# Optimization experiments

Measured on AMD Instinct MI355X. Metric: run time of the kernel, lower is better.

Reference implementation:

```python
import jax, jax.numpy as jnp
from jax import lax
import numpy as np

KS = 8        # window size
SS = 4        # shift size = KS // 2
HEADS = 4


def _l2n(t, axis):
    # torch F.normalize: x / clamp(||x||_2, min=eps)
    return t / jnp.maximum(jnp.linalg.norm(t, axis=axis, keepdims=True), 1e-12)


def _to_windows(t, heads, ks):
    # 'b (head c) (h kh) (w kw) -> b head (h w) (kh kw) c'
    b, hc, H, W = t.shape
    c = hc // heads
    hW, wW = H // ks, W // ks
    t = t.reshape(b, heads, c, hW, ks, wW, ks)
    t = t.transpose(0, 1, 3, 5, 4, 6, 2)  # b,h,hW,wW,kh,kw,c
    return t.reshape(b, heads, hW * wW, ks * ks, c)


def _from_windows(t, hW, wW, ks):
    # 'b head (h w) (kh kw) c -> b (head c) (h kh) (w kw)'
    b, heads, nW, kk, c = t.shape
    t = t.reshape(b, heads, hW, wW, ks, ks, c)
    t = t.transpose(0, 1, 6, 2, 4, 3, 5)  # b,h,c,hW,kh,wW,kw
    return t.reshape(b, heads * c, hW * ks, wW * ks)


def _talk_conv(attn, w, hW, wW):
    # Conv3d(heads->heads, kernel (3,3,1), padding same) over the (hW, wW, K)
    # grid; kernel size 1 on K means an independent 2D conv per K slot, so we
    # fold K into the batch dim and run a single 2D conv.
    b, heads, nW, a1, a2 = attn.shape
    K = a1 * a2
    t = attn.reshape(b, heads, hW, wW, K).transpose(0, 4, 1, 2, 3)
    t = t.reshape(b * K, heads, hW, wW)
    t = lax.conv_general_dilated(t, w, (1, 1), 'SAME',
                                 dimension_numbers=('NCHW', 'OIHW', 'NCHW'))
    t = t.reshape(b, K, heads, hW, wW).transpose(0, 2, 3, 4, 1)
    return t.reshape(b, heads, nW, a1, a2)


def _shift_mask(H, W, ks, ss):
    # Swin-style shifted-window mask; pure numpy constant (shapes are static).
    img = np.zeros((H, W), np.float32)
    cnt = 0
    for hs in (slice(0, -ks), slice(-ks, -ss), slice(-ss, None)):
        for ws in (slice(0, -ks), slice(-ks, -ss), slice(-ss, None)):
            img[hs, ws] = cnt
            cnt += 1
    win = img.reshape(H // ks, ks, W // ks, ks).transpose(0, 2, 1, 3).reshape(-1, ks * ks)
    diff = win[:, None, :] - win[:, :, None]
    return jnp.asarray(np.where(diff != 0, -100.0, 0.0).astype(np.float32))


def _forward(x, w_quz, w_kv, temperature, r_talking, g_talking,
             b_talking_w, l_talking_w, dw_u_w, project_w, project_out_w,
             sca_w, sca_b):
    b, c, H, W = x.shape
    hW, wW = H // KS, W // KS
    quz = jnp.einsum('oc,bchw->bohw', w_quz, x)
    q, u, z = jnp.split(quz, 3, axis=1)
    kv = jnp.einsum('oc,bchw->bohw', w_kv, x)
    k, v = jnp.split(kv, 2, axis=1)
    # shift = True
    q, k, v = (jnp.roll(t, (-SS, -SS), axis=(-1, -2)) for t in (q, k, v))
    q, k, v = (_to_windows(t, HEADS, KS) for t in (q, k, v))  # b,h,nW,kk,c
    qb, ql, qg, qr = jnp.split(q, 4, axis=-1)
    kb, kl, kg, kr = jnp.split(k, 4, axis=-1)
    vb, vl, vg, vr = jnp.split(v, 4, axis=-1)
    qb, kb = _l2n(qb, -1), _l2n(kb, -1)
    ql, kl = _l2n(ql, -2), _l2n(kl, -2)
    qg, kg = _l2n(qg, -3), _l2n(kg, -3)
    qr, kr = _l2n(qr, -3), _l2n(kr, -3)
    # 4 branches (n=window index, i/j=position-in-window, c/d=per-branch chan)
    attn_b = jnp.einsum('bhnic,bhnjc->bhnij', qb, kb) * temperature[0]
    attn_l = jnp.einsum('bhnic,bhnid->bhncd', ql, kl) * temperature[1]
    attn_g = jnp.einsum('bhnic,bhnid->bhicd', qg, kg) * temperature[2]
    attn_r = jnp.einsum('bhnic,bhnjc->bhcij', qr, kr) * temperature[3]
    # talking heads
    attn_b = _talk_conv(attn_b, b_talking_w, hW, wW)
    attn_l = _talk_conv(attn_l, l_talking_w, hW, wW)
    attn_g = jnp.einsum('hklt,bhkcd->btlcd', g_talking, attn_g)
    attn_r = jnp.einsum('hcdt,bhcij->btdij', r_talking, attn_r)
    # shifted-window mask on the brightness branch
    attn_b = attn_b + _shift_mask(H, W, KS, SS)[None, None]
    attn_b, attn_l, attn_g, attn_r = (jax.nn.softmax(t, axis=-1)
                                      for t in (attn_b, attn_l, attn_g, attn_r))
    # outputs, all arranged to (b,h,n,i,c) before un-windowing
    out_b = jnp.einsum('bhnij,bhnjc->bhnic', attn_b, vb)
    out_l = jnp.einsum('bhncd,bhnid->bhnic', attn_l, vl)
    out_g = jnp.einsum('bhicd,bhnid->bhnic', attn_g, vg)
    out_r = jnp.einsum('bhcij,bhnjc->bhnic', attn_r, vr)
    out = jnp.concatenate([_from_windows(t, hW, wW, KS)
                           for t in (out_b, out_l, out_g, out_r)], axis=1)
    out = jnp.roll(out, (SS, SS), axis=(-1, -2))
    # simplified channel attention (global avg pool + 1x1 conv with bias)
    s = jnp.mean(out, axis=(2, 3))
    s = jnp.einsum('oc,bc->bo', sca_w, s) + sca_b
    out = jnp.einsum('oc,bchw->bohw', project_w, out * s[:, :, None, None])
    dw = lax.conv_general_dilated(u, dw_u_w, (1, 1), 'SAME',
                                  feature_group_count=u.shape[1],
                                  dimension_numbers=('NCHW', 'OIHW', 'NCHW'))
    out = out + dw
    return jnp.einsum('oc,bchw->bohw', project_out_w, out * z)


def setup_inputs() -> dict:
    key = jax.random.key(0)
    ks = jax.random.split(key, 12)
    dim, h_dim = 64, 128
    cd = h_dim // HEADS // 4
    b, H, W = 4, 192, 192
    r = lambda i, shp, s: jax.random.normal(ks[i], shp, jnp.float32) * s
    return {
        'x': jax.random.normal(ks[0], (b, dim, H, W), jnp.float32),
        'w_quz': r(1, (3 * h_dim, dim), 0.1),
        'w_kv': r(2, (2 * h_dim, dim), 0.1),
        'temperature': jnp.ones((4, HEADS, 1, 1, 1), jnp.float32),
        'r_talking': r(3, (HEADS, cd, cd, HEADS), 0.2),
        'g_talking': r(4, (HEADS, KS * KS, KS * KS, HEADS), 0.05),
        'b_talking_w': r(5, (HEADS, HEADS, 3, 3), 0.2),
        'l_talking_w': r(6, (HEADS, HEADS, 3, 3), 0.2),
        'dw_u_w': r(7, (h_dim, 1, 3, 3), 0.2),
        'project_w': r(8, (h_dim, h_dim), 0.08),
        'project_out_w': r(9, (dim, h_dim), 0.08),
        'sca_w': r(10, (h_dim, h_dim), 0.08),
        'sca_b': jnp.zeros((h_dim,), jnp.float32),
    }


def reference(x, w_quz, w_kv, temperature, r_talking, g_talking,
              b_talking_w, l_talking_w, dw_u_w, project_w, project_out_w,
              sca_w, sca_b):
    return _forward(x, w_quz, w_kv, temperature, r_talking, g_talking,
                    b_talking_w, l_talking_w, dw_u_w, project_w,
                    project_out_w, sca_w, sca_b)
```

## Files before the change

kernel.cpp:

```cpp
#include <hip/hip_runtime.h>
#include <hip/hip_fp16.h>
#include <cstdint>
#include <cstddef>

#define BB   4
#define CIN  64
#define HD   128
#define NH   4
#define CHW  32
#define CB   8
#define IMG  192
#define SSH  4
#define NWS  24
#define NWIN 576
#define KK   64
#define HWP  (IMG*IMG)

static const size_t NQK16  = (size_t)NH*NWIN*KK*16;
static const size_t NV32   = (size_t)NH*NWIN*KK*CHW;
static const size_t NGR    = (size_t)NH*KK*NWIN*CB;
static const size_t NSP    = (size_t)HD*HWP;
static const size_t NATTNB = (size_t)NH*NWIN*KK*KK;
static const size_t NATTNL = (size_t)NH*NWIN*64;
static const size_t NATTNG = (size_t)NH*KK*64;
static const size_t NATTNR = (size_t)NH*CB*KK*KK;
static const size_t NPART  = (size_t)8*NATTNR;

__device__ inline float wave_max(float v){
  #pragma unroll
  for (int s=1;s<64;s<<=1) v = fmaxf(v, __shfl_xor(v, s));
  return v;
}
__device__ inline float wave_sum(float v){
  #pragma unroll
  for (int s=1;s<64;s<<=1) v += __shfl_xor(v, s);
  return v;
}
__device__ inline float g8_max(float v){
  v = fmaxf(v, __shfl_xor(v,1)); v = fmaxf(v, __shfl_xor(v,2)); v = fmaxf(v, __shfl_xor(v,4));
  return v;
}
__device__ inline float g8_sum(float v){
  v += __shfl_xor(v,1); v += __shfl_xor(v,2); v += __shfl_xor(v,4);
  return v;
}
__device__ inline int regionc(int y){ return (y < IMG-8) ? 0 : ((y < IMG-4) ? 1 : 2); }

__device__ inline size_t widx(int h,int n,int i,int c){
  return (((size_t)h*NWIN + n)*KK + i)*CHW + c;
}
__device__ inline size_t widx16(int h,int n,int i,int c){
  return (((size_t)h*NWIN + n)*KK + i)*16 + c;
}
__device__ inline size_t gidx(int h,int i,int n,int c){
  return (((size_t)(h*KK + i))*NWIN + n)*CB + c;
}
__device__ inline size_t ridx(int h,int c,int n,int i){
  return (((size_t)(h*CB + c))*NWIN + n)*KK + i;
}

__global__ __launch_bounds__(256) void k1_proj(
    const float* __restrict__ x, const float* __restrict__ wquz, const float* __restrict__ wkv,
    float* __restrict__ qw, float* __restrict__ kw, float* __restrict__ vw,
    float* __restrict__ qg, float* __restrict__ kg,
    float* __restrict__ qr, float* __restrict__ kr,
    float* __restrict__ u, float* __restrict__ zbuf, int bsel)
{
  __shared__ float xs[64][20];
  __shared__ float tb[128][17];
  int blk = blockIdx.x;
  int xc = blk % 12, y = blk / 12;
  int x0 = xc*16;
  int t = threadIdx.x;
  {
    int c = t >> 2, p4 = (t & 3)*4;
    float4 v = *(const float4*)&x[((size_t)(bsel*CIN+c)*IMG + y)*IMG + x0 + p4];
    *(float4*)&xs[c][p4] = v;
  }
  int py  = (y + IMG - SSH) % IMG;
  int kh  = py & 7, hwq = py >> 3;
  int wwA = ((x0 - SSH + IMG) % IMG) >> 3;
  int wwB = x0 >> 3;
  int wwC = (x0 + 8) >> 3;
  int pnA = hwq*NWS + wwA, pnB = hwq*NWS + wwB, pnC = hwq*NWS + wwC;
  int piA = kh*8 + 4, piB = kh*8, piC = kh*8;
  #define PN_(p) ((p)<4 ? pnA : ((p)<12 ? pnB : pnC))
  #define PI_(p) ((p)<4 ? (piA+(p)) : ((p)<12 ? (piB+(p)-4) : (piC+(p)-12)))
  __syncthreads();

  int o;
  if (t < 64)       o = (t>>4)*32 + (t&15);
  else if (t < 96)  o = ((t-64)>>3)*32 + 16 + (t&7);
  else if (t < 128) o = ((t-96)>>3)*32 + 24 + (t&7);
  else              o = t;

  {
    const float* wr = wquz + (size_t)o*CIN;
    float acc[16];
    #pragma unroll
    for (int p = 0; p < 16; ++p) acc[p] = 0.f;
    for (int cc = 0; cc < 64; cc += 4){
      float4 w4 = *(const float4*)(wr + cc);
      #pragma unroll
      for (int p = 0; p < 16; ++p){
        acc[p] += w4.x * xs[cc  ][p];
        acc[p] += w4.y * xs[cc+1][p];
        acc[p] += w4.z * xs[cc+2][p];
        acc[p] += w4.w * xs[cc+3][p];
      }
    }
    if (t < 64){
      int h = t >> 4, c = t & 15;
      #pragma unroll
      for (int p = 0; p < 16; ++p) qw[widx16(h,PN_(p),PI_(p),c)] = acc[p];
    } else if (t < 96){
      int h = (t-64) >> 3, cg = t & 7;
      #pragma unroll
      for (int p = 0; p < 16; ++p) qg[gidx(h,PI_(p),PN_(p),cg)] = acc[p];
    } else if (t < 128){
      int h = (t-96) >> 3, cr = t & 7;
      *(float4*)&qr[ridx(h,cr,pnA,piA)]   = make_float4(acc[0],acc[1],acc[2],acc[3]);
      *(float4*)&qr[ridx(h,cr,pnB,piB)]   = make_float4(acc[4],acc[5],acc[6],acc[7]);
      *(float4*)&qr[ridx(h,cr,pnB,piB+4)] = make_float4(acc[8],acc[9],acc[10],acc[11]);
      *(float4*)&qr[ridx(h,cr,pnC,piC)]   = make_float4(acc[12],acc[13],acc[14],acc[15]);
    } else {
      int ch = o - 128;
      #pragma unroll
      for (int p = 0; p < 16; ++p) tb[ch][p] = acc[p];
    }
  }
  __syncthreads();
  {
    int px = t & 15, chg = t >> 4;
    size_t ub = (size_t)y*IMG + x0 + px;
    #pragma unroll
    for (int cc = 0; cc < 8; ++cc){
      int ch = chg*8 + cc;
      u[(size_t)ch*HWP + ub] = tb[ch][px];
    }
  }

  {
    const float* wr = wkv + (size_t)o*CIN;
    float acc[16];
    #pragma unroll
    for (int p = 0; p < 16; ++p) acc[p] = 0.f;
    for (int cc = 0; cc < 64; cc += 4){
      float4 w4 = *(const float4*)(wr + cc);
      #pragma unroll
      for (int p = 0; p < 16; ++p){
        acc[p] += w4.x * xs[cc  ][p];
        acc[p] += w4.y * xs[cc+1][p];
        acc[p] += w4.z * xs[cc+2][p];
        acc[p] += w4.w * xs[cc+3][p];
      }
    }
    if (t < 64){
      int h = t >> 4, c = t & 15;
      #pragma unroll
      for (int p = 0; p < 16; ++p) kw[widx16(h,PN_(p),PI_(p),c)] = acc[p];
    } else if (t < 96){
      int h = (t-64) >> 3, cg = t & 7;
      #pragma unroll
      for (int p = 0; p < 16; ++p) kg[gidx(h,PI_(p),PN_(p),cg)] = acc[p];
    } else if (t < 128){
      int h = (t-96) >> 3, cr = t & 7;
      *(float4*)&kr[ridx(h,cr,pnA,piA)]   = make_float4(acc[0],acc[1],acc[2],acc[3]);
      *(float4*)&kr[ridx(h,cr,pnB,piB)]   = make_float4(acc[4],acc[5],acc[6],acc[7]);
      *(float4*)&kr[ridx(h,cr,pnB,piB+4)] = make_float4(acc[8],acc[9],acc[10],acc[11]);
      *(float4*)&kr[ridx(h,cr,pnC,piC)]   = make_float4(acc[12],acc[13],acc[14],acc[15]);
    } else {
      int oc = o - 128; int h = oc >> 5, c = oc & 31;
      #pragma unroll
      for (int p = 0; p < 16; ++p) vw[widx(h,PN_(p),PI_(p),c)] = acc[p];
    }
  }

  __syncthreads();
  {
    int zr = t >> 1, ph = t & 1;
    const float* wr = wquz + (size_t)(256 + zr)*CIN;
    int pb = ph*8;
    float acc[8];
    #pragma unroll
    for (int p = 0; p < 8; ++p) acc[p] = 0.f;
    for (int cc = 0; cc < 64; cc += 4){
      float4 w4 = *(const float4*)(wr + cc);
      #pragma unroll
      for (int p = 0; p < 8; ++p){
        acc[p] += w4.x * xs[cc  ][pb+p];
        acc[p] += w4.y * xs[cc+1][pb+p];
        acc[p] += w4.z * xs[cc+2][pb+p];
        acc[p] += w4.w * xs[cc+3][pb+p];
      }
    }
    #pragma unroll
    for (int p = 0; p < 8; ++p) tb[zr][pb+p] = acc[p];
  }
  __syncthreads();
  {
    int px = t & 15, chg = t >> 4;
    size_t zb = (size_t)y*IMG + x0 + px;
    #pragma unroll
    for (int cc = 0; cc < 8; ++cc){
      int ch = chg*8 + cc;
      zbuf[(size_t)ch*HWP + zb] = tb[ch][px];
    }
  }
  #undef PN_
  #undef PI_
}

__global__ __launch_bounds__(256) void kA(
    const float* __restrict__ qw, const float* __restrict__ kw,
    const float* __restrict__ qg, const float* __restrict__ kg,
    const float* __restrict__ qr, const float* __restrict__ kr,
    const float* __restrict__ temp,
    __half* __restrict__ attnB, float* __restrict__ attnL,
    float* __restrict__ attnG, float* __restrict__ part,
    float* __restrict__ invqr, float* __restrict__ invkr)
{
  __shared__ __align__(16) char smem[36864];
  int blk = blockIdx.x;
  int t = threadIdx.x;

  if (blk < 576){
    float (*qs)[64][8] = (float(*)[64][8])smem;
    int wv = t >> 6, j = t & 63;
    int gid = blk*4 + wv;
    int n = gid % NWIN, h = gid / NWIN;
    size_t base = widx16(h,n,j,0);
    float q8[CB], k8[CB];
    float sq = 0.f, sk2 = 0.f;
    #pragma unroll
    for (int c = 0; c < CB; ++c){
      q8[c] = qw[base+c]; sq += q8[c]*q8[c];
      k8[c] = kw[base+c]; sk2 += k8[c]*k8[c];
    }
    float invq = 1.f/fmaxf(sqrtf(sq),1e-12f), invk = 1.f/fmaxf(sqrtf(sk2),1e-12f);
    #pragma unroll
    for (int c = 0; c < CB; ++c){ qs[wv][j][c] = q8[c]*invq; k8[c] *= invk; }
    __syncthreads();
    float tmp = temp[h];
    __half* orow = attnB + (size_t)gid*KK*KK;
    for (int i = 0; i < KK; ++i){
      float a = 0.f;
      #pragma unroll
      for (int c = 0; c < CB; ++c) a += qs[wv][i][c]*k8[c];
      orow[(size_t)i*KK + j] = __float2half(a * tmp);
    }
  } else if (blk < 1152){
    int b2 = blk - 576;
    float (*qs)[64][8] = (float(*)[64][8])smem;
    float (*ks)[64][8] = (float(*)[64][8])(smem + 8192);
    float (*invqA)[8] = (float(*)[8])(smem + 16384);
    float (*invkA)[8] = (float(*)[8])(smem + 16384 + 128);
    int wv = t >> 6, tl = t & 63;
    int gid = b2*4 + wv;
    int n = gid % NWIN, h = gid / NWIN;
    size_t base = widx16(h,n,tl,8);
    #pragma unroll
    for (int c = 0; c < CB; ++c){ qs[wv][tl][c] = qw[base+c]; ks[wv][tl][c] = kw[base+c]; }
    __syncthreads();
    int c8 = tl & 7, ig = tl >> 3;
    float sq = 0.f, sk2 = 0.f;
    for (int i = ig; i < KK; i += 8){
      float a = qs[wv][i][c8]; sq += a*a;
      float b = ks[wv][i][c8]; sk2 += b*b;
    }
    #pragma unroll
    for (int m = 8; m < 64; m <<= 1){ sq += __shfl_xor(sq,m); sk2 += __shfl_xor(sk2,m); }
    if (tl < 8){ invqA[wv][tl] = 1.f/fmaxf(sqrtf(sq),1e-12f); invkA[wv][tl] = 1.f/fmaxf(sqrtf(sk2),1e-12f); }
    __syncthreads();
    int c = tl >> 3, d = tl & 7;
    float a = 0.f;
    for (int i = 0; i < KK; ++i) a += qs[wv][i][c]*ks[wv][i][d];
    attnL[(size_t)gid*64 + tl] = a * invqA[wv][c] * invkA[wv][d] * temp[NH + h];
  } else if (blk < 1408){
    int b2 = blk - 1152;
    int i = b2 & 63, h = b2 >> 6;
    float* sq = (float*)smem;
    float* sk = sq + 512;
    float (*redA)[64] = (float(*)[64])(smem + 4096);
    float (*redQ)[64] = (float(*)[64])(smem + 4096 + 1024);
    float (*redK)[64] = (float(*)[64])(smem + 4096 + 2048);
    size_t base = ((size_t)(h*KK+i))*NWIN*CB;
    int np = t >> 6, cd = t & 63, c = cd >> 3, d = cd & 7;
    float a = 0.f, qs2 = 0.f, ks2 = 0.f;
    for (int n0 = 0; n0 < NWIN; n0 += 64){
      __syncthreads();
      for (int idx = t; idx < 512; idx += 256){
        sq[idx] = qg[base + (size_t)n0*CB + idx];
        sk[idx] = kg[base + (size_t)n0*CB + idx];
      }
      __syncthreads();
      for (int nn = np; nn < 64; nn += 4){
        float qv = sq[nn*8+c], kv = sk[nn*8+d];
        a += qv*kv; qs2 += qv*qv; ks2 += kv*kv;
      }
    }
    __syncthreads();
    redA[np][cd] = a; redQ[np][cd] = qs2; redK[np][cd] = ks2;
    __syncthreads();
    if (t < 64){
      float at = redA[0][t]+redA[1][t]+redA[2][t]+redA[3][t];
      float qt = redQ[0][t]+redQ[1][t]+redQ[2][t]+redQ[3][t];
      float kt = redK[0][t]+redK[1][t]+redK[2][t]+redK[3][t];
      at *= (1.f/fmaxf(sqrtf(qt),1e-12f)) * (1.f/fmaxf(sqrtf(kt),1e-12f)) * temp[2*NH + h];
      attnG[(size_t)(h*KK+i)*64 + t] = at;
    }
  } else if (blk < 1664){
    int b2 = blk - 1408;
    int chunk = b2 >> 5, hc = b2 & 31;
    int n0 = chunk*72;
    float* sq = (float*)smem;
    float* sk = sq + 72*64;
    size_t base = (size_t)hc*NWIN*KK + (size_t)n0*KK;
    for (int idx = t; idx < 72*64/4; idx += 256){
      *(float4*)&sq[idx*4] = *(const float4*)&qr[base + (size_t)idx*4];
      *(float4*)&sk[idx*4] = *(const float4*)&kr[base + (size_t)idx*4];
    }
    __syncthreads();
    int j = t & 63, ig = t >> 6;
    float acc[16];
    #pragma unroll
    for (int p = 0; p < 16; ++p) acc[p] = 0.f;
    for (int nn = 0; nn < 72; ++nn){
      float kv = sk[nn*64+j];
      #pragma unroll
      for (int p = 0; p < 16; ++p) acc[p] += sq[nn*64 + ig*16 + p]*kv;
    }
    float* ob = part + (size_t)b2*4096;
    #pragma unroll
    for (int p = 0; p < 16; ++p) ob[(size_t)(ig*16+p)*64 + j] = acc[p];
  } else {
    int hc = blk - 1664;
    float (*rq)[64] = (float(*)[64])smem;
    float (*rk)[64] = (float(*)[64])(smem + 1024);
    size_t base = (size_t)hc*NWIN*KK;
    int i = t & 63, ng = t >> 6;
    float sq = 0.f, sk2 = 0.f;
    for (int n = ng; n < NWIN; n += 4){
      float a = qr[base + (size_t)n*KK + i]; sq  += a*a;
      float b = kr[base + (size_t)n*KK + i]; sk2 += b*b;
    }
    rq[ng][i] = sq; rk[ng][i] = sk2;
    __syncthreads();
    if (t < 64){
      float s = rq[0][t]+rq[1][t]+rq[2][t]+rq[3][t];
      invqr[hc*KK + t] = 1.f/fmaxf(sqrtf(s),1e-12f);
    } else if (t < 128){
      int i2 = t - 64;
      float s = rk[0][i2]+rk[1][i2]+rk[2][i2]+rk[3][i2];
      invkr[hc*KK + i2] = 1.f/fmaxf(sqrtf(s),1e-12f);
    }
  }
}

__global__ __launch_bounds__(256) void kB(
    const __half* __restrict__ attnB, const float* __restrict__ btw,
    const float* __restrict__ vw, float* __restrict__ outa,
    const float* __restrict__ attnL, const float* __restrict__ ltw,
    const float* __restrict__ attnG, const float* __restrict__ gtalk,
    float* __restrict__ attnGp,
    const float* __restrict__ part, const float* __restrict__ invqr,
    const float* __restrict__ invkr, const float* __restrict__ temp,
    float* __restrict__ attnR,
    const float* __restrict__ u, const float* __restrict__ dww,
    float* __restrict__ dwu)
{
  __shared__ __align__(16) char smem[12800];
  int blk = blockIdx.x;
  int t = threadIdx.x;

  if (blk < 9216){
    float (*pbuf)[4][66] = (float(*)[4][66])smem;
    float (*vv)[8][66]   = (float(*)[8][66])(smem + 4224);
    int ig = blk / NWIN, n = blk % NWIN;
    int i0 = ig*4;
    int hw = n / NWS, ww = n % NWS;
    int w = t >> 6, l = t & 63;
    {
      size_t vb = widx(w, n, l, 0);
      float4 va = *(const float4*)&vw[vb];
      float4 vb4 = *(const float4*)&vw[vb + 4];
      vv[w][0][l] = va.x;  vv[w][1][l] = va.y;  vv[w][2][l] = va.z;  vv[w][3][l] = va.w;
      vv[w][4][l] = vb4.x; vv[w][5][l] = vb4.y; vv[w][6][l] = vb4.z; vv[w][7][l] = vb4.w;
    }
    int i = i0 + w;
    float a0 = 0.f, a1 = 0.f, a2 = 0.f, a3 = 0.f;
    #pragma unroll
    for (int nb = 0; nb < 9; ++nb){
      const int dy = nb/3 - 1, dx = nb%3 - 1;
      int hw2 = hw + dy, ww2 = ww + dx;
      if (hw2 >= 0 && hw2 < NWS && ww2 >= 0 && ww2 < NWS){
        int n2 = hw2*NWS + ww2;
        #pragma unroll
        for (int h = 0; h < 4; ++h){
          float r = __half2float(attnB[((size_t)(h*NWIN + n2)*KK + i)*KK + l]);
          a0 += btw[(0*4 + h)*9 + nb] * r;
          a1 += btw[(1*4 + h)*9 + nb] * r;
          a2 += btw[(2*4 + h)*9 + nb] * r;
          a3 += btw[(3*4 + h)*9 + nb] * r;
        }
      }
    }
    int kh = i >> 3, kwd = i & 7;
    int cntI = regionc(hw*8 + kh)*3 + regionc(ww*8 + kwd);
    int cntJ = regionc(hw*8 + (l>>3))*3 + regionc(ww*8 + (l&7));
    float mval = (cntI != cntJ) ? -100.f : 0.f;
    a0 += mval; a1 += mval; a2 += mval; a3 += mval;
    {
      float m0 = wave_max(a0); float e0 = __expf(a0 - m0); pbuf[0][w][l] = e0 / wave_sum(e0);
      float m1 = wave_max(a1); float e1 = __expf(a1 - m1); pbuf[1][w][l] = e1 / wave_sum(e1);
      float m2 = wave_max(a2); float e2 = __expf(a2 - m2); pbuf[2][w][l] = e2 / wave_sum(e2);
      float m3 = wave_max(a3); float e3 = __expf(a3 - m3); pbuf[3][w][l] = e3 / wave_sum(e3);
    }
    __syncthreads();
    {
      int i2 = l >> 4, c = (l >> 1) & 7, jq = l & 1;
      const float* pr = &pbuf[w][i2][jq*32];
      const float* vr = &vv[w][c][jq*32];
      float s = 0.f;
      #pragma unroll
      for (int q = 0; q < 32; ++q) s += pr[q] * vr[q];
      s += __shfl_xor(s, 1);
      if (jq == 0){
        int ii = i0 + i2;
        int khh = ii >> 3, kww = ii & 7;
        int Y = (hw*8 + khh + SSH) % IMG;
        int X = (ww*8 + kww + SSH) % IMG;
        outa[((size_t)(w*CB + c)*HWP) + (size_t)Y*IMG + X] = s;
      }
    }
  } else if (blk < 9792){
    int n = blk - 9216;
    int hw = n/NWS, ww = n%NWS;
    float (*rows)[9][64] = (float(*)[9][64])smem;
    float* wt = (float*)(smem + 9216);
    float (*P)[8][8] = (float(*)[8][8])(smem + 9792);
    if (t < NH*NH*9) wt[t] = ltw[t];
    for (int l = t; l < NH*9*64; l += 256){
      int h = l/(9*64); int nb = (l/64)%9; int cd = l & 63;
      int dy = nb/3-1, dx = nb%3-1; int hw2 = hw+dy, ww2 = ww+dx;
      float v = 0.f;
      if (hw2>=0 && hw2<NWS && ww2>=0 && ww2<NWS)
        v = attnL[((size_t)h*NWIN + hw2*NWS + ww2)*64 + cd];
      rows[h][nb][cd] = v;
    }
    __syncthreads();
    int tt = t >> 6; int cd = t & 63; int c = cd >> 3, d = cd & 7;
    float a = 0.f;
    #pragma unroll
    for (int h = 0; h < NH; ++h)
      #pragma unroll
      for (int nb = 0; nb < 9; ++nb)
        a += wt[(tt*NH + h)*9 + nb] * rows[h][nb][cd];
    float m = g8_max(a);
    float e = __expf(a - m);
    P[tt][c][d] = e / g8_sum(e);
    __syncthreads();
    int i = t & 63;
    size_t vbase = widx(tt, n, i, 8);
    float vl[CB];
    #pragma unroll
    for (int d2 = 0; d2 < CB; ++d2) vl[d2] = vw[vbase + d2];
    int kh = i>>3, kwd = i&7;
    int Y = (hw*8+kh+SSH)%IMG, X = (ww*8+kwd+SSH)%IMG;
    #pragma unroll
    for (int c2 = 0; c2 < CB; ++c2){
      float o = 0.f;
      #pragma unroll
      for (int d2 = 0; d2 < CB; ++d2) o += P[tt][c2][d2]*vl[d2];
      outa[((size_t)(32 + tt*CB + c2)*IMG + Y)*IMG + X] = o;
    }
  } else if (blk < 9856){
    int bb = blk - 9792;
    int w = t >> 6, cd = t & 63;
    int idx = bb*4 + w;
    int l = idx & 63, t2 = idx >> 6;
    float a = 0.f;
    for (int h = 0; h < NH; ++h)
      for (int k = 0; k < KK; ++k)
        a += gtalk[((size_t)(h*KK + k)*KK + l)*NH + t2] * attnG[((size_t)h*KK + k)*64 + cd];
    float m = g8_max(a);
    float e = __expf(a - m);
    attnGp[((size_t)t2*KK + l)*64 + cd] = e / g8_sum(e);
  } else if (blk < 10368){
    int e = (blk - 9856)*256 + t;
    float s = 0.f;
    #pragma unroll
    for (int ch = 0; ch < 8; ++ch) s += part[(size_t)ch*NATTNR + e];
    int hc = e >> 12, ij = e & 4095, i = ij >> 6, j = ij & 63;
    attnR[e] = s * invqr[hc*64+i] * invkr[hc*64+j] * temp[3*NH + (hc>>3)];
  } else {
    int bb = blk - 10368;
    int ch = bb / 48; int y0 = (bb % 48) * 4;
    float (*rows)[192] = (float(*)[192])smem;
    for (int idx = t; idx < 6*48; idx += 256){
      int r = idx / 48, px4 = (idx % 48)*4;
      int yy = y0 - 1 + r;
      float4 v = {0.f,0.f,0.f,0.f};
      if (yy >= 0 && yy < IMG) v = *(const float4*)&u[(size_t)ch*HWP + (size_t)yy*IMG + px4];
      rows[r][px4] = v.x; rows[r][px4+1] = v.y; rows[r][px4+2] = v.z; rows[r][px4+3] = v.w;
    }
    float kw9[9];
    #pragma unroll
    for (int q = 0; q < 9; ++q) kw9[q] = dww[ch*9 + q];
    __syncthreads();
    int r = t >> 6, lane = t & 63;
    for (int kx = 0; kx < 3; ++kx){
      int px = lane + kx*64;
      float s = 0.f;
      #pragma unroll
      for (int dy = 0; dy < 3; ++dy){
        #pragma unroll
        for (int dx = -1; dx <= 1; ++dx){
          int xx = px + dx;
          if (xx >= 0 && xx < IMG) s += kw9[dy*3 + dx + 1] * rows[r+dy][xx];
        }
      }
      dwu[(size_t)ch*HWP + (size_t)(y0+r)*IMG + px] = s;
    }
  }
}

__global__ __launch_bounds__(256) void kC(
    const float* __restrict__ attnGp, const float* __restrict__ vw,
    float* __restrict__ outa,
    const float* __restrict__ attnR, const float* __restrict__ rtalk,
    float* __restrict__ attnRp)
{
  __shared__ __align__(16) char smem[16512];
  int blk = blockIdx.x;
  int t = threadIdx.x;

  if (blk < 2304){
    float* P = (float*)smem;
    int n = blk % NWIN; int t2 = blk / NWIN;
    for (int l = t; l < KK*64; l += 256) P[l] = attnGp[(size_t)t2*KK*64 + l];
    __syncthreads();
    int i = t >> 2; int c0 = (t & 3)*2;
    size_t vbase = widx(t2, n, i, 16);
    float vg[8];
    #pragma unroll
    for (int d = 0; d < 8; ++d) vg[d] = vw[vbase + d];
    int hw = n/NWS, ww = n%NWS; int kh = i>>3, kwd = i&7;
    int Y = (hw*8+kh+SSH)%IMG, X = (ww*8+kwd+SSH)%IMG;
    for (int c = c0; c < c0+2; ++c){
      float o = 0.f;
      #pragma unroll
      for (int d = 0; d < 8; ++d) o += P[(i*8 + c)*8 + d]*vg[d];
      outa[((size_t)(64 + t2*CB + c)*IMG + Y)*IMG + X] = o;
    }
  } else {
    int bb = blk - 2304;
    int d = bb % CB; int t2 = bb / CB;
    float (*S)[64] = (float(*)[64])smem;
    float* wr2 = (float*)(smem + 16384);
    if (t < 32){ int h = t >> 3, c = t & 7; wr2[t] = rtalk[((size_t)(h*CB + c)*CB + d)*NH + t2]; }
    __syncthreads();
    int j = t & 63; int ig = t >> 6;
    float acc[16];
    #pragma unroll
    for (int p = 0; p < 16; ++p) acc[p] = 0.f;
    for (int hc = 0; hc < 32; ++hc){
      float w = wr2[hc];
      const float* Ar = attnR + (size_t)hc*KK*KK;
      #pragma unroll
      for (int p = 0; p < 16; ++p) acc[p] += w * Ar[(size_t)(ig*16+p)*KK + j];
    }
    #pragma unroll
    for (int p = 0; p < 16; ++p) S[ig*16+p][j] = acc[p];
    __syncthreads();
    for (int r = ig; r < 64; r += 4){
      float a = S[r][j];
      float m = wave_max(a);
      float e = __expf(a - m);
      attnRp[(((size_t)t2*CB + d)*KK + r)*KK + j] = e / wave_sum(e);
    }
  }
}

__global__ __launch_bounds__(256) void k7c(
    const float* __restrict__ attnRp, const float* __restrict__ vw, float* __restrict__ outa)
{
  int n = blockIdx.x % NWIN; int t2 = blockIdx.x / NWIN;
  __shared__ float vr[KK][CB];
  int t = threadIdx.x;
  for (int l = t; l < KK*CB; l += 256){
    int j = l >> 3, c = l & 7;
    vr[j][c] = vw[widx(t2, n, j, 24 + c)];
  }
  __syncthreads();
  int i = t & 63; int cg = t >> 6;
  int hw = n/NWS, ww = n%NWS; int kh = i>>3, kwd = i&7;
  int Y = (hw*8+kh+SSH)%IMG, X = (ww*8+kwd+SSH)%IMG;
  for (int c = cg*2; c < cg*2+2; ++c){
    const float* Pr = attnRp + (((size_t)t2*CB + c)*KK + i)*KK;
    float o = 0.f;
    for (int j = 0; j < KK; ++j) o += Pr[j]*vr[j][c];
    outa[((size_t)(96 + t2*CB + c)*IMG + Y)*IMG + X] = o;
  }
}

__global__ __launch_bounds__(256) void k8_mean(const float* __restrict__ outa, float* __restrict__ meanb){
  int ch = blockIdx.x;
  const float4* p = (const float4*)(outa + (size_t)ch*HWP);
  float s = 0.f;
  for (int l = threadIdx.x; l < HWP/4; l += 256){
    float4 v = p[l]; s += v.x+v.y+v.z+v.w;
  }
  __shared__ float red[256];
  red[threadIdx.x] = s; __syncthreads();
  for (int k = 128; k > 0; k >>= 1){
    if (threadIdx.x < k) red[threadIdx.x] += red[threadIdx.x + k];
    __syncthreads();
  }
  if (threadIdx.x == 0) meanb[ch] = red[0] / (float)HWP;
}

#define PADX 68
__global__ __launch_bounds__(256) void k9a(
    const float* __restrict__ outa, const float* __restrict__ meanb,
    const float* __restrict__ scaw, const float* __restrict__ scab,
    const float* __restrict__ projw, const float* __restrict__ dwu,
    const float* __restrict__ zbuf, float* __restrict__ out2z)
{
  __shared__ float WT[128][128];
  __shared__ float xsv[128][PADX];
  __shared__ float sv[128];
  int t = threadIdx.x;
  if (t < 128){
    float s = scab[t];
    const float* srow = scaw + (size_t)t*HD;
    for (int c = 0; c < HD; c += 4){
      float4 w = *(const float4*)&srow[c];
      float4 mm = *(const float4*)&meanb[c];
      s += w.x*mm.x + w.y*mm.y + w.z*mm.z + w.w*mm.w;
    }
    sv[t] = s;
  }
  for (int idx = t; idx < 4096; idx += 256){
    int o = idx & 127; int c4 = (idx >> 7) * 4;
    float4 w = *(const float4*)&projw[(size_t)o*HD + c4];
    WT[c4][o] = w.x; WT[c4+1][o] = w.y; WT[c4+2][o] = w.z; WT[c4+3][o] = w.w;
  }
  int px4 = (t & 15) * 4; int og8 = (t >> 4) * 8;
  for (int tile = 0; tile < 2; ++tile){
    int tid = blockIdx.x * 2 + tile;
    int y = tid / 3, x0 = (tid % 3) * 64;
    size_t sb = (size_t)y*IMG + x0;
    __syncthreads();
    for (int idx = t; idx < 2048; idx += 256){
      int c = idx >> 4; int p4 = (idx & 15) * 4;
      float4 v = *(const float4*)&outa[(size_t)c*HWP + sb + p4];
      float s = sv[c];
      xsv[c][p4] = v.x*s; xsv[c][p4+1] = v.y*s; xsv[c][p4+2] = v.z*s; xsv[c][p4+3] = v.w*s;
    }
    __syncthreads();
    float acc[8][4];
    #pragma unroll
    for (int a = 0; a < 8; ++a){ acc[a][0]=0.f; acc[a][1]=0.f; acc[a][2]=0.f; acc[a][3]=0.f; }
    for (int c = 0; c < 128; ++c){
      float4 xv = *(const float4*)&xsv[c][px4];
      float4 wA = *(const float4*)&WT[c][og8];
      float4 wB = *(const float4*)&WT[c][og8+4];
      float w8[8] = {wA.x,wA.y,wA.z,wA.w,wB.x,wB.y,wB.z,wB.w};
      #pragma unroll
      for (int a = 0; a < 8; ++a){
        acc[a][0] += w8[a]*xv.x; acc[a][1] += w8[a]*xv.y;
        acc[a][2] += w8[a]*xv.z; acc[a][3] += w8[a]*xv.w;
      }
    }
    #pragma unroll
    for (int oo = 0; oo < 8; ++oo){
      int o = og8 + oo;
      size_t off = (size_t)o*HWP + sb + px4;
      float4 d = *(const float4*)&dwu[off];
      float4 z = *(const float4*)&zbuf[off];
      float4 r;
      r.x = (acc[oo][0]+d.x)*z.x; r.y = (acc[oo][1]+d.y)*z.y;
      r.z = (acc[oo][2]+d.z)*z.z; r.w = (acc[oo][3]+d.w)*z.w;
      *(float4*)&out2z[off] = r;
    }
  }
}

__global__ __launch_bounds__(256) void k9b(
    const float* __restrict__ out2z, const float* __restrict__ projow,
    float* __restrict__ dout, int bsel)
{
  __shared__ float WT2[128][64];
  __shared__ float xsv[128][PADX];
  int t = threadIdx.x;
  for (int idx = t; idx < 2048; idx += 256){
    int o = idx & 63; int c4 = (idx >> 6) * 4;
    float4 w = *(const float4*)&projow[(size_t)o*HD + c4];
    WT2[c4][o] = w.x; WT2[c4+1][o] = w.y; WT2[c4+2][o] = w.z; WT2[c4+3][o] = w.w;
  }
  int px4 = (t & 15) * 4; int og4 = (t >> 4) * 4;
  for (int tile = 0; tile < 2; ++tile){
    int tid = blockIdx.x * 2 + tile;
    int y = tid / 3, x0 = (tid % 3) * 64;
    size_t sb = (size_t)y*IMG + x0;
    __syncthreads();
    for (int idx = t; idx < 2048; idx += 256){
      int c = idx >> 4; int p4 = (idx & 15) * 4;
      float4 v = *(const float4*)&out2z[(size_t)c*HWP + sb + p4];
      xsv[c][p4] = v.x; xsv[c][p4+1] = v.y; xsv[c][p4+2] = v.z; xsv[c][p4+3] = v.w;
    }
    __syncthreads();
    float acc[4][4];
    #pragma unroll
    for (int a = 0; a < 4; ++a){ acc[a][0]=0.f; acc[a][1]=0.f; acc[a][2]=0.f; acc[a][3]=0.f; }
    for (int c = 0; c < 128; ++c){
      float4 xv = *(const float4*)&xsv[c][px4];
      float4 w4 = *(const float4*)&WT2[c][og4];
      float w4a[4] = {w4.x,w4.y,w4.z,w4.w};
      #pragma unroll
      for (int a = 0; a < 4; ++a){
        acc[a][0] += w4a[a]*xv.x; acc[a][1] += w4a[a]*xv.y;
        acc[a][2] += w4a[a]*xv.z; acc[a][3] += w4a[a]*xv.w;
      }
    }
    #pragma unroll
    for (int oo = 0; oo < 4; ++oo){
      int o = og4 + oo;
      float4 r; r.x = acc[oo][0]; r.y = acc[oo][1]; r.z = acc[oo][2]; r.w = acc[oo][3];
      *(float4*)&dout[(size_t)(bsel*CIN + o)*HWP + sb + px4] = r;
    }
  }
}

extern "C" void kernel_launch(void* const* d_in, const int* in_sizes, int n_in,
                              void* d_out, int out_size, void* d_ws, size_t ws_size,
                              hipStream_t stream)
{
  const float* x     = (const float*)d_in[0];
  const float* wquz  = (const float*)d_in[1];
  const float* wkv   = (const float*)d_in[2];
  const float* temp  = (const float*)d_in[3];
  const float* rtalk = (const float*)d_in[4];
  const float* gtalk = (const float*)d_in[5];
  const float* btw   = (const float*)d_in[6];
  const float* ltw   = (const float*)d_in[7];
  const float* dww   = (const float*)d_in[8];
  const float* projw = (const float*)d_in[9];
  const float* projow= (const float*)d_in[10];
  const float* scaw  = (const float*)d_in[11];
  const float* scab  = (const float*)d_in[12];
  float* dout = (float*)d_out;

  float* ws = (float*)d_ws;
  float* qw    = ws;
  float* kw    = qw + NQK16;
  float* vw    = kw + NQK16;
  float* qg    = vw + NV32;
  float* kg    = qg + NGR;
  float* qr    = kg + NGR;
  float* kr    = qr + NGR;
  float* u     = kr + NGR;
  float* zbuf  = u + NSP;
  float* outa  = zbuf + NSP;
  float* attnBf= outa + NSP;
  __half* attnBh = (__half*)attnBf;
  float* attnL = attnBf + NSP;
  float* attnG = attnL + NATTNL;
  float* attnGp= attnG + NATTNG;
  float* part  = attnGp + NATTNG;
  float* attnR = part + NPART;
  float* attnRp= attnR + NATTNR;
  float* invqr = attnRp + NATTNR;
  float* invkr = invqr + 2048;
  float* meanb = invkr + 2048;
  float* dwu   = qw;
  float* out2z = attnBf;

  for (int b = 0; b < BB; ++b){
    k1_proj<<<IMG*12, 256, 0, stream>>>(x, wquz, wkv, qw, kw, vw, qg, kg, qr, kr, u, zbuf, b);

    kA<<<1696, 256, 0, stream>>>(qw, kw, qg, kg, qr, kr, temp,
                                 attnBh, attnL, attnG, part, invqr, invkr);

    kB<<<16512, 256, 0, stream>>>(attnBh, btw, vw, outa, attnL, ltw,
                                  attnG, gtalk, attnGp, part, invqr, invkr, temp, attnR,
                                  u, dww, dwu);

    kC<<<2336, 256, 0, stream>>>(attnGp, vw, outa, attnR, rtalk, attnRp);

    k7c<<<NH*NWIN, 256, 0, stream>>>(attnRp, vw, outa);

    k8_mean<<<HD, 256, 0, stream>>>(outa, meanb);

    k9a<<<288, 256, 0, stream>>>(outa, meanb, scaw, scab, projw, dwu, zbuf, out2z);
    k9b<<<288, 256, 0, stream>>>(out2z, projow, dout, b);
  }
}
```

Baseline: 1.194 ms.

## Fuse k1 projection passes and interleave attnB heads for packed loads

The projection kernel now computes the q/k/z (or u/v) outputs in a single pass over the shared x tile, with several accumulator sets per thread, instead of three separate passes. It also drops the half-occupied z pass. The fp16 attention buffer attnB is relaid out with the head index innermost, so the talking-heads conv can fetch all four heads of one element with a single 8-byte load rather than four scattered 2-byte loads. The trade-off is higher register pressure in k1 and less coalesced strided fp16 stores when kA writes attnB.

Measured after the change: 1.320 ms. 1.11x slower.

```diff
diff --git a/kernel.cpp b/kernel.cpp
--- a/kernel.cpp
+++ b/kernel.cpp
@@ -57,6 +57,9 @@
 }
 __device__ inline size_t ridx(int h,int c,int n,int i){
   return (((size_t)(h*CB + c))*NWIN + n)*KK + i;
+}
+__device__ inline size_t bidx(int n,int i,int j,int h){
+  return ((((size_t)n*KK + i)*KK + j)*NH) + h;
 }
 
 __global__ __launch_bounds__(256) void k1_proj(
@@ -92,42 +95,60 @@
   if (t < 64)       o = (t>>4)*32 + (t&15);
   else if (t < 96)  o = ((t-64)>>3)*32 + 16 + (t&7);
   else if (t < 128) o = ((t-96)>>3)*32 + 24 + (t&7);
-  else              o = t;
-
-  {
-    const float* wr = wquz + (size_t)o*CIN;
-    float acc[16];
-    #pragma unroll
-    for (int p = 0; p < 16; ++p) acc[p] = 0.f;
+  else              o = t - 128;
+
+  float acc1[16], acc2[16], acc3[16];
+  #pragma unroll
+  for (int p = 0; p < 16; ++p){ acc1[p]=0.f; acc2[p]=0.f; acc3[p]=0.f; }
+
+  if (t < 128){
+    const float* w1 = wquz + (size_t)o*CIN;
+    const float* w2 = wkv  + (size_t)o*CIN;
+    const float* w3 = wquz + (size_t)(256+o)*CIN;
     for (int cc = 0; cc < 64; cc += 4){
-      float4 w4 = *(const float4*)(wr + cc);
-      #pragma unroll
-      for (int p = 0; p < 16; ++p){
-        acc[p] += w4.x * xs[cc  ][p];
-        acc[p] += w4.y * xs[cc+1][p];
-        acc[p] += w4.z * xs[cc+2][p];
-        acc[p] += w4.w * xs[cc+3][p];
-      }
-    }
-    if (t < 64){
-      int h = t >> 4, c = t & 15;
-      #pragma unroll
-      for (int p = 0; p < 16; ++p) qw[widx16(h,PN_(p),PI_(p),c)] = acc[p];
-    } else if (t < 96){
-      int h = (t-64) >> 3, cg = t & 7;
-      #pragma unroll
-      for (int p = 0; p < 16; ++p) qg[gidx(h,PI_(p),PN_(p),cg)] = acc[p];
-    } else if (t < 128){
-      int h = (t-96) >> 3, cr = t & 7;
-      *(float4*)&qr[ridx(h,cr,pnA,piA)]   = make_float4(acc[0],acc[1],acc[2],acc[3]);
-      *(float4*)&qr[ridx(h,cr,pnB,piB)]   = make_float4(acc[4],acc[5],acc[6],acc[7]);
-      *(float4*)&qr[ridx(h,cr,pnB,piB+4)] = make_float4(acc[8],acc[9],acc[10],acc[11]);
-      *(float4*)&qr[ridx(h,cr,pnC,piC)]   = make_float4(acc[12],acc[13],acc[14],acc[15]);
-    } else {
-      int ch = o - 128;
-      #pragma unroll
-      for (int p = 0; p < 16; ++p) tb[ch][p] = acc[p];
-    }
+      float4 W1 = *(const float4*)(w1+cc);
+      float4 W2 = *(const float4*)(w2+cc);
+      float4 W3 = *(const float4*)(w3+cc);
+      float w1a[4]={W1.x,W1.y,W1.z,W1.w};
+      float w2a[4]={W2.x,W2.y,W2.z,W2.w};
+      float w3a[4]={W3.x,W3.y,W3.z,W3.w};
+      #pragma unroll
+      for (int j = 0; j < 4; ++j){
+        float f1=w1a[j], f2=w2a[j], f3=w3a[j];
+        #pragma unroll
+        for (int q = 0; q < 4; ++q){
+          float4 xv = *(const float4*)&xs[cc+j][q*4];
+          acc1[q*4+0]+=f1*xv.x; acc1[q*4+1]+=f1*xv.y; acc1[q*4+2]+=f1*xv.z; acc1[q*4+3]+=f1*xv.w;
+          acc2[q*4+0]+=f2*xv.x; acc2[q*4+1]+=f2*xv.y; acc2[q*4+2]+=f2*xv.z; acc2[q*4+3]+=f2*xv.w;
+          acc3[q*4+0]+=f3*xv.x; acc3[q*4+1]+=f3*xv.y; acc3[q*4+2]+=f3*xv.z; acc3[q*4+3]+=f3*xv.w;
+        }
+      }
+    }
+  } else {
+    const float* w1 = wquz + (size_t)(o+128)*CIN;
+    const float* w2 = wkv  + (size_t)(o+128)*CIN;
+    for (int cc = 0; cc < 64; cc += 4){
+      float4 W1 = *(const float4*)(w1+cc);
+      float4 W2 = *(const float4*)(w2+cc);
+      float w1a[4]={W1.x,W1.y,W1.z,W1.w};
+      float w2a[4]={W2.x,W2.y,W2.z,W2.w};
+      #pragma unroll
+      for (int j = 0; j < 4; ++j){
+        float f1=w1a[j], f2=w2a[j];
+        #pragma unroll
+        for (int q = 0; q < 4; ++q){
+          float4 xv = *(const float4*)&xs[cc+j][q*4];
+          acc1[q*4+0]+=f1*xv.x; acc1[q*4+1]+=f1*xv.y; acc1[q*4+2]+=f1*xv.z; acc1[q*4+3]+=f1*xv.w;
+          acc2[q*4+0]+=f2*xv.x; acc2[q*4+1]+=f2*xv.y; acc2[q*4+2]+=f2*xv.z; acc2[q*4+3]+=f2*xv.w;
+        }
+      }
+    }
+  }
+
+  if (t >= 128){
+    int ch = t - 128;
+    #pragma unroll
+    for (int p = 0; p < 16; ++p) tb[ch][p] = acc1[p];
   }
   __syncthreads();
   {
@@ -139,63 +160,37 @@
       u[(size_t)ch*HWP + ub] = tb[ch][px];
     }
   }
-
-  {
-    const float* wr = wkv + (size_t)o*CIN;
-    float acc[16];
-    #pragma unroll
-    for (int p = 0; p < 16; ++p) acc[p] = 0.f;
-    for (int cc = 0; cc < 64; cc += 4){
-      float4 w4 = *(const float4*)(wr + cc);
-      #pragma unroll
-      for (int p = 0; p < 16; ++p){
-        acc[p] += w4.x * xs[cc  ][p];
-        acc[p] += w4.y * xs[cc+1][p];
-        acc[p] += w4.z * xs[cc+2][p];
-        acc[p] += w4.w * xs[cc+3][p];
-      }
-    }
-    if (t < 64){
-      int h = t >> 4, c = t & 15;
-      #pragma unroll
-      for (int p = 0; p < 16; ++p) kw[widx16(h,PN_(p),PI_(p),c)] = acc[p];
-    } else if (t < 96){
-      int h = (t-64) >> 3, cg = t & 7;
-      #pragma unroll
-      for (int p = 0; p < 16; ++p) kg[gidx(h,PI_(p),PN_(p),cg)] = acc[p];
-    } else if (t < 128){
-      int h = (t-96) >> 3, cr = t & 7;
-      *(float4*)&kr[ridx(h,cr,pnA,piA)]   = make_float4(acc[0],acc[1],acc[2],acc[3]);
-      *(float4*)&kr[ridx(h,cr,pnB,piB)]   = make_float4(acc[4],acc[5],acc[6],acc[7]);
-      *(float4*)&kr[ridx(h,cr,pnB,piB+4)] = make_float4(acc[8],acc[9],acc[10],acc[11]);
-      *(float4*)&kr[ridx(h,cr,pnC,piC)]   = make_float4(acc[12],acc[13],acc[14],acc[15]);
-    } else {
-      int oc = o - 128; int h = oc >> 5, c = oc & 31;
-      #pragma unroll
-      for (int p = 0; p < 16; ++p) vw[widx(h,PN_(p),PI_(p),c)] = acc[p];
-    }
-  }
-
+  if (t < 64){
+    int h = t >> 4, c = t & 15;
+    #pragma unroll
+    for (int p = 0; p < 16; ++p) qw[widx16(h,PN_(p),PI_(p),c)] = acc1[p];
+    #pragma unroll
+    for (int p = 0; p < 16; ++p) kw[widx16(h,PN_(p),PI_(p),c)] = acc2[p];
+  } else if (t < 96){
+    int h = (t-64) >> 3, cg = t & 7;
+    #pragma unroll
+    for (int p = 0; p < 16; ++p) qg[gidx(h,PI_(p),PN_(p),cg)] = acc1[p];
+    #pragma unroll
+    for (int p = 0; p < 16; ++p) kg[gidx(h,PI_(p),PN_(p),cg)] = acc2[p];
+  } else if (t < 128){
+    int h = (t-96) >> 3, cr = t & 7;
+    *(float4*)&qr[ridx(h,cr,pnA,piA)]   = make_float4(acc1[0],acc1[1],acc1[2],acc1[3]);
+    *(float4*)&qr[ridx(h,cr,pnB,piB)]   = make_float4(acc1[4],acc1[5],acc1[6],acc1[7]);
+    *(float4*)&qr[ridx(h,cr,pnB,piB+4)] = make_float4(acc1[8],acc1[9],acc1[10],acc1[11]);
+    *(float4*)&qr[ridx(h,cr,pnC,piC)]   = make_float4(acc1[12],acc1[13],acc1[14],acc1[15]);
+    *(float4*)&kr[ridx(h,cr,pnA,piA)]   = make_float4(acc2[0],acc2[1],acc2[2],acc2[3]);
+    *(float4*)&kr[ridx(h,cr,pnB,piB)]   = make_float4(acc2[4],acc2[5],acc2[6],acc2[7]);
+    *(float4*)&kr[ridx(h,cr,pnB,piB+4)] = make_float4(acc2[8],acc2[9],acc2[10],acc2[11]);
+    *(float4*)&kr[ridx(h,cr,pnC,piC)]   = make_float4(acc2[12],acc2[13],acc2[14],acc2[15]);
+  } else {
+    int ch = t - 128; int h = ch >> 5, c = ch & 31;
+    #pragma unroll
+    for (int p = 0; p < 16; ++p) vw[widx(h,PN_(p),PI_(p),c)] = acc2[p];
+  }
   __syncthreads();
-  {
-    int zr = t >> 1, ph = t & 1;
-    const float* wr = wquz + (size_t)(256 + zr)*CIN;
-    int pb = ph*8;
-    float acc[8];
-    #pragma unroll
-    for (int p = 0; p < 8; ++p) acc[p] = 0.f;
-    for (int cc = 0; cc < 64; cc += 4){
-      float4 w4 = *(const float4*)(wr + cc);
-      #pragma unroll
-      for (int p = 0; p < 8; ++p){
-        acc[p] += w4.x * xs[cc  ][pb+p];
-        acc[p] += w4.y * xs[cc+1][pb+p];
-        acc[p] += w4.z * xs[cc+2][pb+p];
-        acc[p] += w4.w * xs[cc+3][pb+p];
-      }
-    }
-    #pragma unroll
-    for (int p = 0; p < 8; ++p) tb[zr][pb+p] = acc[p];
+  if (t < 128){
+    #pragma unroll
+    for (int p = 0; p < 16; ++p) tb[o][p] = acc3[p];
   }
   __syncthreads();
   {
@@ -226,9 +221,8 @@
 
   if (blk < 576){
     float (*qs)[64][8] = (float(*)[64][8])smem;
-    int wv = t >> 6, j = t & 63;
-    int gid = blk*4 + wv;
-    int n = gid % NWIN, h = gid / NWIN;
+    int h = t >> 6, j = t & 63;
+    int n = blk;
     size_t base = widx16(h,n,j,0);
     float q8[CB], k8[CB];
     float sq = 0.f, sk2 = 0.f;
@@ -239,15 +233,14 @@
     }
     float invq = 1.f/fmaxf(sqrtf(sq),1e-12f), invk = 1.f/fmaxf(sqrtf(sk2),1e-12f);
     #pragma unroll
-    for (int c = 0; c < CB; ++c){ qs[wv][j][c] = q8[c]*invq; k8[c] *= invk; }
+    for (int c = 0; c < CB; ++c){ qs[h][j][c] = q8[c]*invq; k8[c] *= invk; }
     __syncthreads();
     float tmp = temp[h];
-    __half* orow = attnB + (size_t)gid*KK*KK;
     for (int i = 0; i < KK; ++i){
       float a = 0.f;
       #pragma unroll
-      for (int c = 0; c < CB; ++c) a += qs[wv][i][c]*k8[c];
-      orow[(size_t)i*KK + j] = __float2half(a * tmp);
+      for (int c = 0; c < CB; ++c) a += qs[h][i][c]*k8[c];
+      attnB[bidx(n,i,j,h)] = __float2half(a * tmp);
     }
   } else if (blk < 1152){
     int b2 = blk - 576;
@@ -395,14 +388,20 @@
       int hw2 = hw + dy, ww2 = ww + dx;
       if (hw2 >= 0 && hw2 < NWS && ww2 >= 0 && ww2 < NWS){
         int n2 = hw2*NWS + ww2;
-        #pragma unroll
-        for (int h = 0; h < 4; ++h){
-          float r = __half2float(attnB[((size_t)(h*NWIN + n2)*KK + i)*KK + l]);
-          a0 += btw[(0*4 + h)*9 + nb] * r;
-          a1 += btw[(1*4 + h)*9 + nb] * r;
-          a2 += btw[(2*4 + h)*9 + nb] * r;
-          a3 += btw[(3*4 + h)*9 + nb] * r;
-        }
+        const uint2* pb = (const uint2*)(attnB + bidx(n2, i, 0, 0));
+        uint2 pk = pb[l];
+        __half2 p01 = *reinterpret_cast<__half2*>(&pk.x);
+        __half2 p23 = *reinterpret_cast<__half2*>(&pk.y);
+        float2 f01 = __half22float2(p01);
+        float2 f23 = __half22float2(p23);
+        a0 += btw[0*36 + 0*9 + nb]*f01.x + btw[0*36 + 1*9 + nb]*f01.y
+            + btw[0*36 + 2*9 + nb]*f23.x + btw[0*36 + 3*9 + nb]*f23.y;
+        a1 += btw[1*36 + 0*9 + nb]*f01.x + btw[1*36 + 1*9 + nb]*f01.y
+            + btw[1*36 + 2*9 + nb]*f23.x + btw[1*36 + 3*9 + nb]*f23.y;
+        a2 += btw[2*36 + 0*9 + nb]*f01.x + btw[2*36 + 1*9 + nb]*f01.y
+            + btw[2*36 + 2*9 + nb]*f23.x + btw[2*36 + 3*9 + nb]*f23.y;
+        a3 += btw[3*36 + 0*9 + nb]*f01.x + btw[3*36 + 1*9 + nb]*f01.y
+            + btw[3*36 + 2*9 + nb]*f23.x + btw[3*36 + 3*9 + nb]*f23.y;
       }
     }
     int kh = i >> 3, kwd = i & 7;
```
